# Performance work log

Measured on AMD Instinct MI355X. Metric: run time of the kernel, lower is better.

Reference implementation:

```python
import jax, jax.numpy as jnp
import numpy as np

K = 5  # k_neighbors


def _pairwise_sq(a, b):
    # (B,N,3),(B,M,3) -> (B,N,M) squared euclidean distances (matmul form)
    d = (jnp.sum(a * a, -1)[:, :, None] + jnp.sum(b * b, -1)[:, None, :]
         - 2.0 * jnp.einsum('bnd,bmd->bnm', a, b))
    return jnp.maximum(d, 0.0)


def _knn_indices(points, k):
    # (B,N,3) -> (B,N,k) indices of k nearest neighbors, excluding self
    d = _pairwise_sq(points, points)
    _, idx = jax.lax.top_k(-d, k + 1)
    return idx[:, :, 1:]


def _gather_neighbors(feats, idx):
    # feats (B,N,C), idx (B,N,k) -> (B,N,k,C)
    B, N, k = idx.shape
    flat = jnp.take_along_axis(feats, idx.reshape(B, N * k, 1), axis=1)
    return flat.reshape(B, N, k, feats.shape[-1])


def setup_inputs() -> dict:
    key = jax.random.key(0)
    ks = jax.random.split(key, 8)
    B, N, M = 8, 4096, 4000
    return {
        'Y': jax.random.normal(ks[0], (B, N, 3), jnp.float32),
        'X': jax.random.normal(ks[1], (B, M, 3), jnp.float32),
        'R_pred': jax.random.normal(ks[2], (B, 3, 3), jnp.float32),
        't_pred': jax.random.normal(ks[3], (B, 3), jnp.float32),
        'R_gt': jax.random.normal(ks[4], (B, 3, 3), jnp.float32),
        't_gt': jax.random.normal(ks[5], (B, 3), jnp.float32),
        'X_hat': jax.random.normal(ks[6], (B, N, 3), jnp.float32),
        'delta': jax.random.normal(ks[7], (B, N, 3), jnp.float32),
    }


def reference(Y, X, R_pred, t_pred, R_gt, t_gt, X_hat, delta):
    lam_rot, lam_trans, lam_rmse = 1.0, 1.0, 1.0
    lam_align, lam_disp, lam_deform, lam_lap = 1.0, 0.01, 0.1, 0.1

    # --- rigid losses ---
    # rotation geodesic: R_delta = R_pred^T @ R_gt
    R_delta = jnp.einsum('bij,bik->bjk', R_pred, R_gt)
    tr = jnp.trace(R_delta, axis1=1, axis2=2)
    cos_a = jnp.clip((tr - 1.0) / 2.0, -1.0 + 1e-7, 1.0 - 1e-7)
    L_rot = jnp.mean(jnp.arccos(cos_a))

    L_trans = jnp.mean(jnp.linalg.norm(t_pred - t_gt, axis=1))

    # Y @ R^T + t
    Y_pred = jnp.einsum('bnd,bkd->bnk', Y, R_pred) + t_pred[:, None, :]
    Y_gt = jnp.einsum('bnd,bkd->bnk', Y, R_gt) + t_gt[:, None, :]
    L_rmse = jnp.mean(jnp.sqrt(jnp.mean(jnp.sum((Y_pred - Y_gt) ** 2, -1), axis=1)))

    rigid = lam_rot * L_rot + lam_trans * L_trans + lam_rmse * L_rmse

    # --- non-rigid losses ---
    Y_rigid = Y_pred  # apply_rigid_transform(Y, R_pred, t_pred)

    # alignment: N != M -> kNN matching of X_hat against X
    d_align = _pairwise_sq(X_hat, X)          # (B,N,M)
    knn_d = -jax.lax.top_k(-d_align, K)[0]    # (B,N,K) smallest distances
    L_align = jnp.mean(knn_d)

    L_disp = jnp.mean(jnp.sum(delta ** 2, -1))

    # kNN graph on Y_rigid (original builds it twice with identical result)
    idx = _knn_indices(Y_rigid, K)            # (B,N,K)

    Yn = _gather_neighbors(Y_rigid, idx)      # (B,N,K,3)
    Xn = _gather_neighbors(X_hat, idx)
    edge_diff = (Xn - X_hat[:, :, None, :]) - (Yn - Y_rigid[:, :, None, :])
    L_deform = jnp.mean(jnp.sum(edge_diff ** 2, -1))

    dn = _gather_neighbors(delta, idx)        # (B,N,K,3)
    lap = delta - jnp.mean(dn, axis=2)
    L_lap = jnp.mean(jnp.sum(lap ** 2, -1))

    non_rigid = (lam_align * L_align + lam_disp * L_disp
                 + lam_deform * L_deform + lam_lap * L_lap)
    total = rigid + non_rigid

    return jnp.stack([total, rigid, non_rigid, L_rot, L_trans, L_rmse,
                      L_align, L_disp, L_deform, L_lap])
```

## Files before the change

### kernel.cpp

```cpp
#include <hip/hip_runtime.h>
#include <math.h>

#define BB 8
#define NN 4096
#define MM 4000
#define KK 5
#define NWAVE 8
#define QG 128
#define CH 512
#define NPAD 4096
#define SCAN_BLOCKS ((NN / QG) * BB * 2)

#define ACC_ROT    0
#define ACC_TRANS  1
#define ACC_ALIGN  2
#define ACC_DISP   3
#define ACC_DEFORM 4
#define ACC_LAP    5
#define ACC_RMSE   6
#define ACC_COUNT  14

#define INFF __int_as_float(0x7F800000)

__device__ __forceinline__ float waveReduceSum(float v) {
#pragma unroll
    for (int off = 32; off > 0; off >>= 1) v += __shfl_down(v, off, 64);
    return v;
}

template<bool SELF, bool PACK>
__device__ __forceinline__ void proc1(float4 c, int midx, int q,
                                      float ca, float cbq, float cc,
                                      float& b0, float& b1, float& b2,
                                      float& b3, float& b4) {
    float sc = fmaf(c.x, ca, fmaf(c.y, cbq, fmaf(c.z, cc, c.w)));
    float v;
    if (PACK) {
        unsigned pk = (__float_as_uint(sc) & 0xFFFFF000u) | (unsigned)midx;
        v = __uint_as_float(pk);
        if (SELF) v = (midx == q) ? INFF : v;
    } else {
        v = sc;
    }
    float n0 = fminf(b0, v);
    float n1 = __builtin_amdgcn_fmed3f(v, b0, b1);
    float n2 = __builtin_amdgcn_fmed3f(v, b1, b2);
    float n3 = __builtin_amdgcn_fmed3f(v, b2, b3);
    float n4 = __builtin_amdgcn_fmed3f(v, b3, b4);
    b0 = n0; b1 = n1; b2 = n2; b3 = n3; b4 = n4;
}

template<bool SELF, bool PACK>
__device__ __forceinline__ void scanLDS2(const float4* lc, int tc,
                                         float a0, float b0c, float c0, int q0,
                                         float a1, float b1c, float c1, int q1,
                                         float& x0, float& x1, float& x2,
                                         float& x3, float& x4,
                                         float& y0, float& y1, float& y2,
                                         float& y3, float& y4) {
    float4 A[4], B[4];
#pragma unroll
    for (int j = 0; j < 4; ++j) A[j] = lc[tc + j];

    for (int t0 = 0; t0 < CH; t0 += 8) {
#pragma unroll
        for (int j = 0; j < 4; ++j) B[j] = lc[tc + t0 + 4 + j];
#pragma unroll
        for (int j = 0; j < 4; ++j) {
            proc1<SELF, PACK>(A[j], tc + t0 + j, q0, a0, b0c, c0, x0, x1, x2, x3, x4);
            proc1<SELF, PACK>(A[j], tc + t0 + j, q1, a1, b1c, c1, y0, y1, y2, y3, y4);
        }
        if (t0 + 8 < CH) {
#pragma unroll
            for (int j = 0; j < 4; ++j) A[j] = lc[tc + t0 + 8 + j];
        }
#pragma unroll
        for (int j = 0; j < 4; ++j) {
            proc1<SELF, PACK>(B[j], tc + t0 + 4 + j, q0, a0, b0c, c0, x0, x1, x2, x3, x4);
            proc1<SELF, PACK>(B[j], tc + t0 + 4 + j, q1, a1, b1c, c1, y0, y1, y2, y3, y4);
        }
    }
}

__global__ void k_prep(const float* __restrict__ Y, const float* __restrict__ X,
                       const float* __restrict__ Rp, const float* __restrict__ tp,
                       const float* __restrict__ Rg, const float* __restrict__ tg,
                       const float* __restrict__ dl,
                       float4* __restrict__ YrP, float4* __restrict__ XP,
                       float* __restrict__ acc) {
    int b = blockIdx.x >> 4;
    int n = ((blockIdx.x & 15) << 8) + threadIdx.x;
    size_t base = ((size_t)b * NN + n) * 3;
    float yx = Y[base + 0], yy = Y[base + 1], yz = Y[base + 2];

    float rp[9], rg[9], tpv[3], tgv[3];
#pragma unroll
    for (int i = 0; i < 9; ++i) { rp[i] = Rp[b * 9 + i]; rg[i] = Rg[b * 9 + i]; }
#pragma unroll
    for (int i = 0; i < 3; ++i) { tpv[i] = tp[b * 3 + i]; tgv[i] = tg[b * 3 + i]; }

    float p[3], dr2 = 0.f;
#pragma unroll
    for (int k = 0; k < 3; ++k) {
        float pv = fmaf(yx, rp[k * 3 + 0], fmaf(yy, rp[k * 3 + 1], fmaf(yz, rp[k * 3 + 2], tpv[k])));
        float gv = fmaf(yx, rg[k * 3 + 0], fmaf(yy, rg[k * 3 + 1], fmaf(yz, rg[k * 3 + 2], tgv[k])));
        p[k] = pv;
        float dd = pv - gv;
        dr2 = fmaf(dd, dd, dr2);
    }
    YrP[(size_t)b * NPAD + n] =
        make_float4(p[0], p[1], p[2], fmaf(p[0], p[0], fmaf(p[1], p[1], p[2] * p[2])));

    float4 xe;
    if (n < MM) {
        size_t xb = ((size_t)b * MM + n) * 3;
        float x0 = X[xb + 0], x1 = X[xb + 1], x2 = X[xb + 2];
        xe = make_float4(x0, x1, x2, fmaf(x0, x0, fmaf(x1, x1, x2 * x2)));
    } else {
        xe = make_float4(0.f, 0.f, 0.f, INFF);
    }
    XP[(size_t)b * NPAD + n] = xe;

    float d0 = dl[base + 0], d1 = dl[base + 1], d2 = dl[base + 2];
    float dsq = d0 * d0 + d1 * d1 + d2 * d2;

    dr2 = waveReduceSum(dr2);
    dsq = waveReduceSum(dsq);
    if ((threadIdx.x & 63) == 0) {
        atomicAdd(&acc[ACC_RMSE + b], dr2);
        atomicAdd(&acc[ACC_DISP], dsq);
    }

    if (threadIdx.x == 0 && (blockIdx.x & 15) == 0) {
        float tr = 0.f;
#pragma unroll
        for (int i = 0; i < 9; ++i) tr += rp[i] * rg[i];
        float c = (tr - 1.f) * 0.5f;
        c = fminf(fmaxf(c, -1.f + 1e-7f), 1.f - 1e-7f);
        float dx = tpv[0] - tgv[0], dy = tpv[1] - tgv[1], dz = tpv[2] - tgv[2];
        atomicAdd(&acc[ACC_ROT], acosf(c));
        atomicAdd(&acc[ACC_TRANS], sqrtf(dx * dx + dy * dy + dz * dz));
    }
}

__device__ void finalize(const float* acc, float* out) {
    float a[ACC_COUNT];
#pragma unroll
    for (int i = 0; i < ACC_COUNT; ++i)
        a[i] = __hip_atomic_load(&acc[i], __ATOMIC_RELAXED, __HIP_MEMORY_SCOPE_AGENT);
    float L_rot = a[ACC_ROT] / BB;
    float L_trans = a[ACC_TRANS] / BB;
    float L_rmse = 0.f;
#pragma unroll
    for (int b = 0; b < BB; ++b) L_rmse += sqrtf(a[ACC_RMSE + b] / NN);
    L_rmse /= BB;
    float L_align = a[ACC_ALIGN] / ((float)BB * NN * KK);
    float L_disp = a[ACC_DISP] / ((float)BB * NN);
    float L_def = a[ACC_DEFORM] / ((float)BB * NN * KK);
    float L_lap = a[ACC_LAP] / ((float)BB * NN);
    float rigid = L_rot + L_trans + L_rmse;
    float nr = L_align + 0.01f * L_disp + 0.1f * L_def + 0.1f * L_lap;
    out[0] = rigid + nr; out[1] = rigid; out[2] = nr;
    out[3] = L_rot; out[4] = L_trans; out[5] = L_rmse;
    out[6] = L_align; out[7] = L_disp; out[8] = L_def; out[9] = L_lap;
}

#define MERGE_STEP(W) { float d = mdp[((W) * QG + l) * 6 + pp##W]; if (d < best) { best = d; bw = W; } }
#define MERGE_ADV()  { pp0 += (bw == 0); pp1 += (bw == 1); pp2 += (bw == 2); pp3 += (bw == 3); \
                       pp4 += (bw == 4); pp5 += (bw == 5); pp6 += (bw == 6); pp7 += (bw == 7); }

__global__ __launch_bounds__(512, 4) void k_scan(const float* __restrict__ Xh,
                                                 const float4* __restrict__ XP,
                                                 const float4* __restrict__ YrP,
                                                 const float* __restrict__ dl,
                                                 float* __restrict__ acc,
                                                 unsigned* __restrict__ doneCnt,
                                                 float* __restrict__ out) {
    __shared__ float4 lsbuf[NPAD];
    float* mdp = (float*)lsbuf;
    int tid = threadIdx.x, wave = tid >> 6, lane = tid & 63;
    int qg = blockIdx.x, b = blockIdx.y, mode = blockIdx.z;
    int q0 = qg * QG + lane, q1 = q0 + 64;

    const float4* cbG = (mode == 0 ? XP : YrP) + (size_t)b * NPAD;
#pragma unroll
    for (int i = 0; i < NPAD / 512; ++i) lsbuf[tid + i * 512] = cbG[tid + i * 512];

    float qx0, qy0, qz0, qx1, qy1, qz1;
    if (mode == 0) {
        size_t a0 = ((size_t)b * NN + q0) * 3;
        size_t a1 = ((size_t)b * NN + q1) * 3;
        qx0 = Xh[a0 + 0]; qy0 = Xh[a0 + 1]; qz0 = Xh[a0 + 2];
        qx1 = Xh[a1 + 0]; qy1 = Xh[a1 + 1]; qz1 = Xh[a1 + 2];
    } else {
        float4 p0 = cbG[q0], p1 = cbG[q1];
        qx0 = p0.x; qy0 = p0.y; qz0 = p0.z;
        qx1 = p1.x; qy1 = p1.y; qz1 = p1.z;
    }
    __syncthreads();

    float x0 = INFF, x1 = INFF, x2 = INFF, x3 = INFF, x4 = INFF;
    float y0 = INFF, y1 = INFF, y2 = INFF, y3 = INFF, y4 = INFF;
    int tc = wave * CH;
    if (mode == 0) {
        scanLDS2<false, false>(lsbuf, tc,
                               -2.f * qx0, -2.f * qy0, -2.f * qz0, 0,
                               -2.f * qx1, -2.f * qy1, -2.f * qz1, 0,
                               x0, x1, x2, x3, x4, y0, y1, y2, y3, y4);
    } else if (wave == (qg >> 2)) {
        scanLDS2<true, true>(lsbuf, tc,
                             -2.f * qx0, -2.f * qy0, -2.f * qz0, q0,
                             -2.f * qx1, -2.f * qy1, -2.f * qz1, q1,
                             x0, x1, x2, x3, x4, y0, y1, y2, y3, y4);
    } else {
        scanLDS2<false, true>(lsbuf, tc,
                              -2.f * qx0, -2.f * qy0, -2.f * qz0, q0,
                              -2.f * qx1, -2.f * qy1, -2.f * qz1, q1,
                              x0, x1, x2, x3, x4, y0, y1, y2, y3, y4);
    }
    __syncthreads();

    float* m0 = &mdp[(wave * QG + lane) * 6];
    m0[0] = x0; m0[1] = x1; m0[2] = x2; m0[3] = x3; m0[4] = x4; m0[5] = INFF;
    float* m1 = &mdp[(wave * QG + lane + 64) * 6];
    m1[0] = y0; m1[1] = y1; m1[2] = y2; m1[3] = y3; m1[4] = y4; m1[5] = INFF;
    __syncthreads();

    if (tid < QG) {
        int l = tid;
        int q = qg * QG + l;
        int pp0 = 0, pp1 = 0, pp2 = 0, pp3 = 0, pp4 = 0, pp5 = 0, pp6 = 0, pp7 = 0;
        if (mode == 0) {
            size_t a0 = ((size_t)b * NN + q) * 3;
            float qx = Xh[a0 + 0], qy = Xh[a0 + 1], qz = Xh[a0 + 2];
            float qn = fmaf(qx, qx, fmaf(qy, qy, qz * qz));
            float s = 0.f;
#pragma unroll
            for (int k = 0; k < KK; ++k) {
                float best = INFF; int bw = 0;
                MERGE_STEP(0) MERGE_STEP(1) MERGE_STEP(2) MERGE_STEP(3)
                MERGE_STEP(4) MERGE_STEP(5) MERGE_STEP(6) MERGE_STEP(7)
                s += fmaxf(best + qn, 0.f);
                MERGE_ADV()
            }
            s = waveReduceSum(s);
            if ((l & 63) == 0) atomicAdd(&acc[ACC_ALIGN], s);
        } else {
            int si[KK];
#pragma unroll
            for (int k = 0; k < KK; ++k) {
                float best = INFF; int bw = 0;
                MERGE_STEP(0) MERGE_STEP(1) MERGE_STEP(2) MERGE_STEP(3)
                MERGE_STEP(4) MERGE_STEP(5) MERGE_STEP(6) MERGE_STEP(7)
                si[k] = (int)(__float_as_uint(best) & 0xFFFu);
                MERGE_ADV()
            }
            float4 qp = cbG[q];
            const float* xh = Xh + (size_t)b * NN * 3;
            const float* dlb = dl + (size_t)b * NN * 3;
            float xnx = xh[q * 3 + 0], xny = xh[q * 3 + 1], xnz = xh[q * 3 + 2];
            float dnx = dlb[q * 3 + 0], dny = dlb[q * 3 + 1], dnz = dlb[q * 3 + 2];

            float def = 0.f, sx = 0.f, sy = 0.f, sz = 0.f;
#pragma unroll
            for (int k = 0; k < KK; ++k) {
                int n = si[k];
                float4 yj = cbG[n];
                float ex = (xh[n * 3 + 0] - xnx) - (yj.x - qp.x);
                float ey = (xh[n * 3 + 1] - xny) - (yj.y - qp.y);
                float ez = (xh[n * 3 + 2] - xnz) - (yj.z - qp.z);
                def += ex * ex + ey * ey + ez * ez;
                sx += dlb[n * 3 + 0]; sy += dlb[n * 3 + 1]; sz += dlb[n * 3 + 2];
            }
            float lx = dnx - sx / 5.f, ly = dny - sy / 5.f, lz = dnz - sz / 5.f;
            float lap = lx * lx + ly * ly + lz * lz;

            def = waveReduceSum(def);
            lap = waveReduceSum(lap);
            if ((l & 63) == 0) {
                atomicAdd(&acc[ACC_DEFORM], def);
                atomicAdd(&acc[ACC_LAP], lap);
            }
        }
    }
    __syncthreads();
    if (tid == 0) {
        __threadfence();
        unsigned t = __hip_atomic_fetch_add(doneCnt, 1u, __ATOMIC_ACQ_REL,
                                            __HIP_MEMORY_SCOPE_AGENT);
        if (t == SCAN_BLOCKS - 1) finalize(acc, out);
    }
}

extern "C" void kernel_launch(void* const* d_in, const int* in_sizes, int n_in,
                              void* d_out, int out_size, void* d_ws, size_t ws_size,
                              hipStream_t stream) {
    const float* Y  = (const float*)d_in[0];
    const float* X  = (const float*)d_in[1];
    const float* Rp = (const float*)d_in[2];
    const float* tp = (const float*)d_in[3];
    const float* Rg = (const float*)d_in[4];
    const float* tg = (const float*)d_in[5];
    const float* Xh = (const float*)d_in[6];
    const float* dl = (const float*)d_in[7];
    float* out = (float*)d_out;

    float*    acc     = (float*)d_ws;
    unsigned* doneCnt = (unsigned*)((char*)d_ws + 64);
    float4*   YrP     = (float4*)((char*)d_ws + 512);
    float4*   XP      = YrP + (size_t)BB * NPAD;

    hipMemsetAsync(d_ws, 0, 512, stream);
    hipLaunchKernelGGL(k_prep, dim3(BB * NN / 256), dim3(256), 0, stream,
                       Y, X, Rp, tp, Rg, tg, dl, YrP, XP, acc);
    hipLaunchKernelGGL(k_scan, dim3(NN / QG, BB, 2), dim3(512), 0, stream,
                       Xh, XP, YrP, dl, acc, doneCnt, out);
}
```

Measured before the change: 109.7 us.

## Scan candidate points directly from global memory instead of staging through LDS

Drops the block-wide copy of the whole per-batch candidate set into shared memory and its barriers. Each wave now reads its candidate chunk straight from global memory, which is wave-uniform (broadcast) and should hit the cache. The software prefetch depth is doubled from 4 to 8 float4 per stage to hide the longer global latency. Shared memory shrinks to just the merge buffer, which may allow more resident blocks, at the cost of more registers and a dependence on cache behaviour.

```diff
diff --git a/kernel.cpp b/kernel.cpp
--- a/kernel.cpp
+++ b/kernel.cpp
@@ -51,33 +51,33 @@
 }
 
 template<bool SELF, bool PACK>
-__device__ __forceinline__ void scanLDS2(const float4* lc, int tc,
-                                         float a0, float b0c, float c0, int q0,
-                                         float a1, float b1c, float c1, int q1,
-                                         float& x0, float& x1, float& x2,
-                                         float& x3, float& x4,
-                                         float& y0, float& y1, float& y2,
-                                         float& y3, float& y4) {
-    float4 A[4], B[4];
-#pragma unroll
-    for (int j = 0; j < 4; ++j) A[j] = lc[tc + j];
-
-    for (int t0 = 0; t0 < CH; t0 += 8) {
-#pragma unroll
-        for (int j = 0; j < 4; ++j) B[j] = lc[tc + t0 + 4 + j];
-#pragma unroll
-        for (int j = 0; j < 4; ++j) {
+__device__ __forceinline__ void scanGlob2(const float4* __restrict__ cb, int tc,
+                                          float a0, float b0c, float c0, int q0,
+                                          float a1, float b1c, float c1, int q1,
+                                          float& x0, float& x1, float& x2,
+                                          float& x3, float& x4,
+                                          float& y0, float& y1, float& y2,
+                                          float& y3, float& y4) {
+    float4 A[8], B[8];
+#pragma unroll
+    for (int j = 0; j < 8; ++j) A[j] = cb[tc + j];
+
+    for (int t0 = 0; t0 < CH; t0 += 16) {
+#pragma unroll
+        for (int j = 0; j < 8; ++j) B[j] = cb[tc + t0 + 8 + j];
+#pragma unroll
+        for (int j = 0; j < 8; ++j) {
             proc1<SELF, PACK>(A[j], tc + t0 + j, q0, a0, b0c, c0, x0, x1, x2, x3, x4);
             proc1<SELF, PACK>(A[j], tc + t0 + j, q1, a1, b1c, c1, y0, y1, y2, y3, y4);
         }
-        if (t0 + 8 < CH) {
-#pragma unroll
-            for (int j = 0; j < 4; ++j) A[j] = lc[tc + t0 + 8 + j];
+        if (t0 + 16 < CH) {
+#pragma unroll
+            for (int j = 0; j < 8; ++j) A[j] = cb[tc + t0 + 16 + j];
         }
 #pragma unroll
-        for (int j = 0; j < 4; ++j) {
-            proc1<SELF, PACK>(B[j], tc + t0 + 4 + j, q0, a0, b0c, c0, x0, x1, x2, x3, x4);
-            proc1<SELF, PACK>(B[j], tc + t0 + 4 + j, q1, a1, b1c, c1, y0, y1, y2, y3, y4);
+        for (int j = 0; j < 8; ++j) {
+            proc1<SELF, PACK>(B[j], tc + t0 + 8 + j, q0, a0, b0c, c0, x0, x1, x2, x3, x4);
+            proc1<SELF, PACK>(B[j], tc + t0 + 8 + j, q1, a1, b1c, c1, y0, y1, y2, y3, y4);
         }
     }
 }
@@ -165,7 +165,7 @@
     out[6] = L_align; out[7] = L_disp; out[8] = L_def; out[9] = L_lap;
 }
 
-#define MERGE_STEP(W) { float d = mdp[((W) * QG + l) * 6 + pp##W]; if (d < best) { best = d; bw = W; } }
+#define MERGE_STEP(W) { float d = md[W][l][pp##W]; if (d < best) { best = d; bw = W; } }
 #define MERGE_ADV()  { pp0 += (bw == 0); pp1 += (bw == 1); pp2 += (bw == 2); pp3 += (bw == 3); \
                        pp4 += (bw == 4); pp5 += (bw == 5); pp6 += (bw == 6); pp7 += (bw == 7); }
 
@@ -176,15 +176,12 @@
                                                  float* __restrict__ acc,
                                                  unsigned* __restrict__ doneCnt,
                                                  float* __restrict__ out) {
-    __shared__ float4 lsbuf[NPAD];
-    float* mdp = (float*)lsbuf;
+    __shared__ float md[NWAVE][QG][6];
     int tid = threadIdx.x, wave = tid >> 6, lane = tid & 63;
     int qg = blockIdx.x, b = blockIdx.y, mode = blockIdx.z;
     int q0 = qg * QG + lane, q1 = q0 + 64;
 
     const float4* cbG = (mode == 0 ? XP : YrP) + (size_t)b * NPAD;
-#pragma unroll
-    for (int i = 0; i < NPAD / 512; ++i) lsbuf[tid + i * 512] = cbG[tid + i * 512];
 
     float qx0, qy0, qz0, qx1, qy1, qz1;
     if (mode == 0) {
@@ -197,33 +194,32 @@
         qx0 = p0.x; qy0 = p0.y; qz0 = p0.z;
         qx1 = p1.x; qy1 = p1.y; qz1 = p1.z;
     }
-    __syncthreads();
 
     float x0 = INFF, x1 = INFF, x2 = INFF, x3 = INFF, x4 = INFF;
     float y0 = INFF, y1 = INFF, y2 = INFF, y3 = INFF, y4 = INFF;
     int tc = wave * CH;
     if (mode == 0) {
-        scanLDS2<false, false>(lsbuf, tc,
-                               -2.f * qx0, -2.f * qy0, -2.f * qz0, 0,
-                               -2.f * qx1, -2.f * qy1, -2.f * qz1, 0,
-                               x0, x1, x2, x3, x4, y0, y1, y2, y3, y4);
+        scanGlob2<false, false>(cbG, tc,
+                                -2.f * qx0, -2.f * qy0, -2.f * qz0, 0,
+                                -2.f * qx1, -2.f * qy1, -2.f * qz1, 0,
+                                x0, x1, x2, x3, x4, y0, y1, y2, y3, y4);
     } else if (wave == (qg >> 2)) {
-        scanLDS2<true, true>(lsbuf, tc,
-                             -2.f * qx0, -2.f * qy0, -2.f * qz0, q0,
-                             -2.f * qx1, -2.f * qy1, -2.f * qz1, q1,
-                             x0, x1, x2, x3, x4, y0, y1, y2, y3, y4);
-    } else {
-        scanLDS2<false, true>(lsbuf, tc,
+        scanGlob2<true, true>(cbG, tc,
                               -2.f * qx0, -2.f * qy0, -2.f * qz0, q0,
                               -2.f * qx1, -2.f * qy1, -2.f * qz1, q1,
                               x0, x1, x2, x3, x4, y0, y1, y2, y3, y4);
-    }
-    __syncthreads();
-
-    float* m0 = &mdp[(wave * QG + lane) * 6];
-    m0[0] = x0; m0[1] = x1; m0[2] = x2; m0[3] = x3; m0[4] = x4; m0[5] = INFF;
-    float* m1 = &mdp[(wave * QG + lane + 64) * 6];
-    m1[0] = y0; m1[1] = y1; m1[2] = y2; m1[3] = y3; m1[4] = y4; m1[5] = INFF;
+    } else {
+        scanGlob2<false, true>(cbG, tc,
+                               -2.f * qx0, -2.f * qy0, -2.f * qz0, q0,
+                               -2.f * qx1, -2.f * qy1, -2.f * qz1, q1,
+                               x0, x1, x2, x3, x4, y0, y1, y2, y3, y4);
+    }
+
+    md[wave][lane][0] = x0; md[wave][lane][1] = x1; md[wave][lane][2] = x2;
+    md[wave][lane][3] = x3; md[wave][lane][4] = x4; md[wave][lane][5] = INFF;
+    md[wave][lane + 64][0] = y0; md[wave][lane + 64][1] = y1;
+    md[wave][lane + 64][2] = y2; md[wave][lane + 64][3] = y3;
+    md[wave][lane + 64][4] = y4; md[wave][lane + 64][5] = INFF;
     __syncthreads();
 
     if (tid < QG) {
```

Result: slower. 118.5 us (+8.0%).

## Split candidate scan into halves with separate merge kernel

Applied to the files above, without the earlier changes.

The scan kernel now loads only half of the candidate set into LDS per block and doubles the grid, with each wave scanning 256 candidates. Per-half top-5 partial results go to workspace, and a new merge kernel combines the two halves, computes the deform, laplacian and alignment sums, and finalizes. This halves LDS use so more blocks fit per CU (launch bounds raised to 6) and gives more parallelism. In exchange it adds an extra kernel launch and global round-trips for the partial lists.

```diff
diff --git a/kernel.cpp b/kernel.cpp
--- a/kernel.cpp
+++ b/kernel.cpp
@@ -7,9 +7,11 @@
 #define KK 5
 #define NWAVE 8
 #define QG 128
-#define CH 512
+#define CH 256
+#define HSZ 2048
 #define NPAD 4096
-#define SCAN_BLOCKS ((NN / QG) * BB * 2)
+#define MQ_BLK 256
+#define M_BLOCKS (BB * NN / MQ_BLK)
 
 #define ACC_ROT    0
 #define ACC_TRANS  1
@@ -51,7 +53,7 @@
 }
 
 template<bool SELF, bool PACK>
-__device__ __forceinline__ void scanLDS2(const float4* lc, int tc,
+__device__ __forceinline__ void scanLDS2(const float4* lc, int tl, int tg,
                                          float a0, float b0c, float c0, int q0,
                                          float a1, float b1c, float c1, int q1,
                                          float& x0, float& x1, float& x2,
@@ -60,24 +62,24 @@
                                          float& y3, float& y4) {
     float4 A[4], B[4];
 #pragma unroll
-    for (int j = 0; j < 4; ++j) A[j] = lc[tc + j];
+    for (int j = 0; j < 4; ++j) A[j] = lc[tl + j];
 
     for (int t0 = 0; t0 < CH; t0 += 8) {
 #pragma unroll
-        for (int j = 0; j < 4; ++j) B[j] = lc[tc + t0 + 4 + j];
+        for (int j = 0; j < 4; ++j) B[j] = lc[tl + t0 + 4 + j];
 #pragma unroll
         for (int j = 0; j < 4; ++j) {
-            proc1<SELF, PACK>(A[j], tc + t0 + j, q0, a0, b0c, c0, x0, x1, x2, x3, x4);
-            proc1<SELF, PACK>(A[j], tc + t0 + j, q1, a1, b1c, c1, y0, y1, y2, y3, y4);
+            proc1<SELF, PACK>(A[j], tg + t0 + j, q0, a0, b0c, c0, x0, x1, x2, x3, x4);
+            proc1<SELF, PACK>(A[j], tg + t0 + j, q1, a1, b1c, c1, y0, y1, y2, y3, y4);
         }
         if (t0 + 8 < CH) {
 #pragma unroll
-            for (int j = 0; j < 4; ++j) A[j] = lc[tc + t0 + 8 + j];
+            for (int j = 0; j < 4; ++j) A[j] = lc[tl + t0 + 8 + j];
         }
 #pragma unroll
         for (int j = 0; j < 4; ++j) {
-            proc1<SELF, PACK>(B[j], tc + t0 + 4 + j, q0, a0, b0c, c0, x0, x1, x2, x3, x4);
-            proc1<SELF, PACK>(B[j], tc + t0 + 4 + j, q1, a1, b1c, c1, y0, y1, y2, y3, y4);
+            proc1<SELF, PACK>(B[j], tg + t0 + 4 + j, q0, a0, b0c, c0, x0, x1, x2, x3, x4);
+            proc1<SELF, PACK>(B[j], tg + t0 + 4 + j, q1, a1, b1c, c1, y0, y1, y2, y3, y4);
         }
     }
 }
@@ -140,6 +142,86 @@
         float dx = tpv[0] - tgv[0], dy = tpv[1] - tgv[1], dz = tpv[2] - tgv[2];
         atomicAdd(&acc[ACC_ROT], acosf(c));
         atomicAdd(&acc[ACC_TRANS], sqrtf(dx * dx + dy * dy + dz * dz));
+    }
+}
+
+#define MERGE_STEP(W) { float d = mdp[((W) * QG + l) * 6 + pp##W]; if (d < best) { best = d; bw = W; } }
+#define MERGE_ADV()  { pp0 += (bw == 0); pp1 += (bw == 1); pp2 += (bw == 2); pp3 += (bw == 3); \
+                       pp4 += (bw == 4); pp5 += (bw == 5); pp6 += (bw == 6); pp7 += (bw == 7); }
+
+__global__ __launch_bounds__(512, 6) void k_scan(const float* __restrict__ Xh,
+                                                 const float4* __restrict__ XP,
+                                                 const float4* __restrict__ YrP,
+                                                 float* __restrict__ pa,
+                                                 float* __restrict__ pk) {
+    __shared__ float4 lsbuf[HSZ];
+    float* mdp = (float*)lsbuf;
+    int tid = threadIdx.x, wave = tid >> 6, lane = tid & 63;
+    int qg = blockIdx.x, b = blockIdx.y;
+    int half = blockIdx.z & 1, mode = blockIdx.z >> 1;
+    int q0 = qg * QG + lane, q1 = q0 + 64;
+
+    const float4* cbG = (mode == 0 ? XP : YrP) + (size_t)b * NPAD;
+#pragma unroll
+    for (int i = 0; i < HSZ / 512; ++i)
+        lsbuf[tid + i * 512] = cbG[half * HSZ + tid + i * 512];
+
+    float qx0, qy0, qz0, qx1, qy1, qz1;
+    if (mode == 0) {
+        size_t a0 = ((size_t)b * NN + q0) * 3;
+        size_t a1 = ((size_t)b * NN + q1) * 3;
+        qx0 = Xh[a0 + 0]; qy0 = Xh[a0 + 1]; qz0 = Xh[a0 + 2];
+        qx1 = Xh[a1 + 0]; qy1 = Xh[a1 + 1]; qz1 = Xh[a1 + 2];
+    } else {
+        float4 p0 = cbG[q0], p1 = cbG[q1];
+        qx0 = p0.x; qy0 = p0.y; qz0 = p0.z;
+        qx1 = p1.x; qy1 = p1.y; qz1 = p1.z;
+    }
+    __syncthreads();
+
+    float x0 = INFF, x1 = INFF, x2 = INFF, x3 = INFF, x4 = INFF;
+    float y0 = INFF, y1 = INFF, y2 = INFF, y3 = INFF, y4 = INFF;
+    int tl = wave * CH;
+    int tg = half * HSZ + tl;
+    bool hasSelf = (mode == 1) && (half == (qg >> 4)) && (wave == ((qg >> 1) & 7));
+    if (mode == 0) {
+        scanLDS2<false, false>(lsbuf, tl, tg,
+                               -2.f * qx0, -2.f * qy0, -2.f * qz0, 0,
+                               -2.f * qx1, -2.f * qy1, -2.f * qz1, 0,
+                               x0, x1, x2, x3, x4, y0, y1, y2, y3, y4);
+    } else if (hasSelf) {
+        scanLDS2<true, true>(lsbuf, tl, tg,
+                             -2.f * qx0, -2.f * qy0, -2.f * qz0, q0,
+                             -2.f * qx1, -2.f * qy1, -2.f * qz1, q1,
+                             x0, x1, x2, x3, x4, y0, y1, y2, y3, y4);
+    } else {
+        scanLDS2<false, true>(lsbuf, tl, tg,
+                              -2.f * qx0, -2.f * qy0, -2.f * qz0, q0,
+                              -2.f * qx1, -2.f * qy1, -2.f * qz1, q1,
+                              x0, x1, x2, x3, x4, y0, y1, y2, y3, y4);
+    }
+    __syncthreads();
+
+    float* m0 = &mdp[(wave * QG + lane) * 6];
+    m0[0] = x0; m0[1] = x1; m0[2] = x2; m0[3] = x3; m0[4] = x4; m0[5] = INFF;
+    float* m1 = &mdp[(wave * QG + lane + 64) * 6];
+    m1[0] = y0; m1[1] = y1; m1[2] = y2; m1[3] = y3; m1[4] = y4; m1[5] = INFF;
+    __syncthreads();
+
+    if (tid < QG) {
+        int l = tid;
+        int q = qg * QG + l;
+        int pp0 = 0, pp1 = 0, pp2 = 0, pp3 = 0, pp4 = 0, pp5 = 0, pp6 = 0, pp7 = 0;
+        float* dst = (mode == 0 ? pa : pk) + (((size_t)b * NN + q) * 2 + half) * 6;
+#pragma unroll
+        for (int k = 0; k < KK; ++k) {
+            float best = INFF; int bw = 0;
+            MERGE_STEP(0) MERGE_STEP(1) MERGE_STEP(2) MERGE_STEP(3)
+            MERGE_STEP(4) MERGE_STEP(5) MERGE_STEP(6) MERGE_STEP(7)
+            dst[k] = best;
+            MERGE_ADV()
+        }
+        dst[5] = INFF;
     }
 }
 
@@ -165,130 +247,77 @@
     out[6] = L_align; out[7] = L_disp; out[8] = L_def; out[9] = L_lap;
 }
 
-#define MERGE_STEP(W) { float d = mdp[((W) * QG + l) * 6 + pp##W]; if (d < best) { best = d; bw = W; } }
-#define MERGE_ADV()  { pp0 += (bw == 0); pp1 += (bw == 1); pp2 += (bw == 2); pp3 += (bw == 3); \
-                       pp4 += (bw == 4); pp5 += (bw == 5); pp6 += (bw == 6); pp7 += (bw == 7); }
-
-__global__ __launch_bounds__(512, 4) void k_scan(const float* __restrict__ Xh,
-                                                 const float4* __restrict__ XP,
-                                                 const float4* __restrict__ YrP,
-                                                 const float* __restrict__ dl,
-                                                 float* __restrict__ acc,
-                                                 unsigned* __restrict__ doneCnt,
-                                                 float* __restrict__ out) {
-    __shared__ float4 lsbuf[NPAD];
-    float* mdp = (float*)lsbuf;
-    int tid = threadIdx.x, wave = tid >> 6, lane = tid & 63;
-    int qg = blockIdx.x, b = blockIdx.y, mode = blockIdx.z;
-    int q0 = qg * QG + lane, q1 = q0 + 64;
-
-    const float4* cbG = (mode == 0 ? XP : YrP) + (size_t)b * NPAD;
-#pragma unroll
-    for (int i = 0; i < NPAD / 512; ++i) lsbuf[tid + i * 512] = cbG[tid + i * 512];
-
-    float qx0, qy0, qz0, qx1, qy1, qz1;
-    if (mode == 0) {
-        size_t a0 = ((size_t)b * NN + q0) * 3;
-        size_t a1 = ((size_t)b * NN + q1) * 3;
-        qx0 = Xh[a0 + 0]; qy0 = Xh[a0 + 1]; qz0 = Xh[a0 + 2];
-        qx1 = Xh[a1 + 0]; qy1 = Xh[a1 + 1]; qz1 = Xh[a1 + 2];
-    } else {
-        float4 p0 = cbG[q0], p1 = cbG[q1];
-        qx0 = p0.x; qy0 = p0.y; qz0 = p0.z;
-        qx1 = p1.x; qy1 = p1.y; qz1 = p1.z;
+__global__ void k_merge(const float4* __restrict__ YrP, const float* __restrict__ Xh,
+                        const float* __restrict__ dl, const float* __restrict__ pa,
+                        const float* __restrict__ pk, float* __restrict__ acc,
+                        unsigned* __restrict__ doneCnt, float* __restrict__ out) {
+    int gid = blockIdx.x * MQ_BLK + threadIdx.x;
+    int b = gid >> 12, q = gid & (NN - 1);
+
+    size_t qb = (size_t)gid * 3;
+    float qhx = Xh[qb + 0], qhy = Xh[qb + 1], qhz = Xh[qb + 2];
+    float qn = fmaf(qhx, qhx, fmaf(qhy, qhy, qhz * qhz));
+    {
+        const float* p0 = pa + (size_t)gid * 12;
+        const float* p1 = p0 + 6;
+        int i = 0, j = 0;
+        float s = 0.f;
+#pragma unroll
+        for (int k = 0; k < KK; ++k) {
+            float a = p0[i], c = p1[j];
+            bool ta = (a <= c);
+            s += fmaxf((ta ? a : c) + qn, 0.f);
+            i += ta; j += !ta;
+        }
+        s = waveReduceSum(s);
+        if ((threadIdx.x & 63) == 0) atomicAdd(&acc[ACC_ALIGN], s);
+    }
+
+    const float4* cb = YrP + (size_t)b * NPAD;
+    float4 qp = cb[q];
+    const float* p0 = pk + (size_t)gid * 12;
+    const float* p1 = p0 + 6;
+    int i = 0, j = 0;
+    int si[KK];
+#pragma unroll
+    for (int k = 0; k < KK; ++k) {
+        float a = p0[i], c = p1[j];
+        bool ta = (a <= c);
+        si[k] = (int)(__float_as_uint(ta ? a : c) & 0xFFFu);
+        i += ta; j += !ta;
+    }
+
+    const float* xh = Xh + (size_t)b * NN * 3;
+    const float* dlb = dl + (size_t)b * NN * 3;
+    float xnx = xh[q * 3 + 0], xny = xh[q * 3 + 1], xnz = xh[q * 3 + 2];
+    float dnx = dlb[q * 3 + 0], dny = dlb[q * 3 + 1], dnz = dlb[q * 3 + 2];
+
+    float def = 0.f, sx = 0.f, sy = 0.f, sz = 0.f;
+#pragma unroll
+    for (int k = 0; k < KK; ++k) {
+        int n = si[k];
+        float4 yj = cb[n];
+        float ex = (xh[n * 3 + 0] - xnx) - (yj.x - qp.x);
+        float ey = (xh[n * 3 + 1] - xny) - (yj.y - qp.y);
+        float ez = (xh[n * 3 + 2] - xnz) - (yj.z - qp.z);
+        def += ex * ex + ey * ey + ez * ez;
+        sx += dlb[n * 3 + 0]; sy += dlb[n * 3 + 1]; sz += dlb[n * 3 + 2];
+    }
+    float lx = dnx - sx / 5.f, ly = dny - sy / 5.f, lz = dnz - sz / 5.f;
+    float lap = lx * lx + ly * ly + lz * lz;
+
+    def = waveReduceSum(def);
+    lap = waveReduceSum(lap);
+    if ((threadIdx.x & 63) == 0) {
+        atomicAdd(&acc[ACC_DEFORM], def);
+        atomicAdd(&acc[ACC_LAP], lap);
     }
     __syncthreads();
-
-    float x0 = INFF, x1 = INFF, x2 = INFF, x3 = INFF, x4 = INFF;
-    float y0 = INFF, y1 = INFF, y2 = INFF, y3 = INFF, y4 = INFF;
-    int tc = wave * CH;
-    if (mode == 0) {
-        scanLDS2<false, false>(lsbuf, tc,
-                               -2.f * qx0, -2.f * qy0, -2.f * qz0, 0,
-                               -2.f * qx1, -2.f * qy1, -2.f * qz1, 0,
-                               x0, x1, x2, x3, x4, y0, y1, y2, y3, y4);
-    } else if (wave == (qg >> 2)) {
-        scanLDS2<true, true>(lsbuf, tc,
-                             -2.f * qx0, -2.f * qy0, -2.f * qz0, q0,
-                             -2.f * qx1, -2.f * qy1, -2.f * qz1, q1,
-                             x0, x1, x2, x3, x4, y0, y1, y2, y3, y4);
-    } else {
-        scanLDS2<false, true>(lsbuf, tc,
-                              -2.f * qx0, -2.f * qy0, -2.f * qz0, q0,
-                              -2.f * qx1, -2.f * qy1, -2.f * qz1, q1,
-                              x0, x1, x2, x3, x4, y0, y1, y2, y3, y4);
-    }
-    __syncthreads();
-
-    float* m0 = &mdp[(wave * QG + lane) * 6];
-    m0[0] = x0; m0[1] = x1; m0[2] = x2; m0[3] = x3; m0[4] = x4; m0[5] = INFF;
-    float* m1 = &mdp[(wave * QG + lane + 64) * 6];
-    m1[0] = y0; m1[1] = y1; m1[2] = y2; m1[3] = y3; m1[4] = y4; m1[5] = INFF;
-    __syncthreads();
-
-    if (tid < QG) {
-        int l = tid;
-        int q = qg * QG + l;
-        int pp0 = 0, pp1 = 0, pp2 = 0, pp3 = 0, pp4 = 0, pp5 = 0, pp6 = 0, pp7 = 0;
-        if (mode == 0) {
-            size_t a0 = ((size_t)b * NN + q) * 3;
-            float qx = Xh[a0 + 0], qy = Xh[a0 + 1], qz = Xh[a0 + 2];
-            float qn = fmaf(qx, qx, fmaf(qy, qy, qz * qz));
-            float s = 0.f;
-#pragma unroll
-            for (int k = 0; k < KK; ++k) {
-                float best = INFF; int bw = 0;
-                MERGE_STEP(0) MERGE_STEP(1) MERGE_STEP(2) MERGE_STEP(3)
-                MERGE_STEP(4) MERGE_STEP(5) MERGE_STEP(6) MERGE_STEP(7)
-                s += fmaxf(best + qn, 0.f);
-                MERGE_ADV()
-            }
-            s = waveReduceSum(s);
-            if ((l & 63) == 0) atomicAdd(&acc[ACC_ALIGN], s);
-        } else {
-            int si[KK];
-#pragma unroll
-            for (int k = 0; k < KK; ++k) {
-                float best = INFF; int bw = 0;
-                MERGE_STEP(0) MERGE_STEP(1) MERGE_STEP(2) MERGE_STEP(3)
-                MERGE_STEP(4) MERGE_STEP(5) MERGE_STEP(6) MERGE_STEP(7)
-                si[k] = (int)(__float_as_uint(best) & 0xFFFu);
-                MERGE_ADV()
-            }
-            float4 qp = cbG[q];
-            const float* xh = Xh + (size_t)b * NN * 3;
-            const float* dlb = dl + (size_t)b * NN * 3;
-            float xnx = xh[q * 3 + 0], xny = xh[q * 3 + 1], xnz = xh[q * 3 + 2];
-            float dnx = dlb[q * 3 + 0], dny = dlb[q * 3 + 1], dnz = dlb[q * 3 + 2];
-
-            float def = 0.f, sx = 0.f, sy = 0.f, sz = 0.f;
-#pragma unroll
-            for (int k = 0; k < KK; ++k) {
-                int n = si[k];
-                float4 yj = cbG[n];
-                float ex = (xh[n * 3 + 0] - xnx) - (yj.x - qp.x);
-                float ey = (xh[n * 3 + 1] - xny) - (yj.y - qp.y);
-                float ez = (xh[n * 3 + 2] - xnz) - (yj.z - qp.z);
-                def += ex * ex + ey * ey + ez * ez;
-                sx += dlb[n * 3 + 0]; sy += dlb[n * 3 + 1]; sz += dlb[n * 3 + 2];
-            }
-            float lx = dnx - sx / 5.f, ly = dny - sy / 5.f, lz = dnz - sz / 5.f;
-            float lap = lx * lx + ly * ly + lz * lz;
-
-            def = waveReduceSum(def);
-            lap = waveReduceSum(lap);
-            if ((l & 63) == 0) {
-                atomicAdd(&acc[ACC_DEFORM], def);
-                atomicAdd(&acc[ACC_LAP], lap);
-            }
-        }
-    }
-    __syncthreads();
-    if (tid == 0) {
+    if (threadIdx.x == 0) {
         __threadfence();
         unsigned t = __hip_atomic_fetch_add(doneCnt, 1u, __ATOMIC_ACQ_REL,
                                             __HIP_MEMORY_SCOPE_AGENT);
-        if (t == SCAN_BLOCKS - 1) finalize(acc, out);
+        if (t == M_BLOCKS - 1) finalize(acc, out);
     }
 }
 
@@ -309,10 +338,14 @@
     unsigned* doneCnt = (unsigned*)((char*)d_ws + 64);
     float4*   YrP     = (float4*)((char*)d_ws + 512);
     float4*   XP      = YrP + (size_t)BB * NPAD;
+    float*    pa      = (float*)(XP + (size_t)BB * NPAD);
+    float*    pk      = pa + (size_t)BB * NN * 12;
 
     hipMemsetAsync(d_ws, 0, 512, stream);
     hipLaunchKernelGGL(k_prep, dim3(BB * NN / 256), dim3(256), 0, stream,
                        Y, X, Rp, tp, Rg, tg, dl, YrP, XP, acc);
-    hipLaunchKernelGGL(k_scan, dim3(NN / QG, BB, 2), dim3(512), 0, stream,
-                       Xh, XP, YrP, dl, acc, doneCnt, out);
-}
+    hipLaunchKernelGGL(k_scan, dim3(NN / QG, BB, 4), dim3(512), 0, stream,
+                       Xh, XP, YrP, pa, pk);
+    hipLaunchKernelGGL(k_merge, dim3(M_BLOCKS), dim3(MQ_BLK), 0, stream,
+                       YrP, Xh, dl, pa, pk, acc, doneCnt, out);
+}
```

After: 115.2 us. +5.0%, slower.
